# Kernel optimization log

Hardware: AMD Instinct MI355X
Metric: run time of the kernel (lower is better)

Reference implementation:

```python
import jax, jax.numpy as jnp
import numpy as np

S = 15      # subject_nums
C = 2048    # in_channels (extractor output dim)
NC = 3      # num_classes
B = 1024    # subject_batch_num (rows per subject)
SUBJ = 7    # target subject
KERNEL_MUL = 2.0
KERNEL_NUM = 5


def setup_inputs() -> dict:
    key = jax.random.key(0)
    k = jax.random.split(key, 5)
    x = jax.random.normal(k[0], (S * B, C), dtype=jnp.float32)
    labels = jax.random.randint(k[1], (S * B,), 0, NC)
    y = jax.nn.one_hot(labels, NC, dtype=jnp.float32)
    subject_label = jnp.repeat(jnp.arange(S, dtype=jnp.int32), B)
    W_add = 0.02 * jax.random.normal(k[2], (S, 512, C), dtype=jnp.float32)
    b_add = jnp.zeros((S, 512), dtype=jnp.float32)
    W_cls = 0.02 * jax.random.normal(k[3], (S, NC, 512), dtype=jnp.float32)
    b_cls = jnp.zeros((S, NC), dtype=jnp.float32)
    return {"x": x, "y": y, "subject_label": subject_label,
            "W_add": W_add, "b_add": b_add, "W_cls": W_cls, "b_cls": b_cls,
            "subject": SUBJ}


def _mmd(source, target):
    # Standard multi-kernel Gaussian MMD (DAN-style), as used in the repo.
    n = source.shape[0]
    total = jnp.concatenate([source, target], axis=0)      # [2n, d]
    sq = jnp.sum(total * total, axis=-1)
    d2 = sq[:, None] + sq[None, :] - 2.0 * (total @ total.T)  # [2n, 2n]
    m = 2 * n
    bandwidth = jnp.sum(d2) / (m * m - m)
    bandwidth = bandwidth / (KERNEL_MUL ** (KERNEL_NUM // 2))
    kernels = sum(jnp.exp(-d2 / (bandwidth * (KERNEL_MUL ** i))) for i in range(KERNEL_NUM))
    XX = kernels[:n, :n]
    YY = kernels[n:, n:]
    XY = kernels[:n, n:]
    YX = kernels[n:, :n]
    return jnp.mean(XX + YY - XY - YX)


def reference(x, y, subject_label, W_add, b_add, W_cls, b_cls, subject):
    S_ = W_add.shape[0]
    b = x.shape[0] // S_          # == (subject_label == subject).sum() by construction
    K = S_ - 1
    idx = np.array([i for i in range(S_) if i != subject])  # static: subject is a Python int

    xr = x.reshape(S_, b, -1)
    src = xr[idx]                 # [K, b, C] source-subject blocks
    tgt = xr[subject]             # [b, C] target-subject block
    Wk, bk = W_add[idx], b_add[idx]

    # Grouped per-subject addblock Linear(C -> 512)
    outs = jnp.einsum('kbc,kdc->kbd', src, Wk) + bk[:, None, :]       # [K, b, 512]
    t_outs = jnp.einsum('bc,kdc->kbd', tgt, Wk) + bk[:, None, :]      # [K, b, 512]

    # Class predictors: ReLU + Linear(512 -> NC), predictors 0..K-1 are used
    Wc, bc = W_cls[:K], b_cls[:K]
    logits = jnp.einsum('kbd,knd->kbn', jax.nn.relu(outs), Wc) + bc[:, None, :]
    t_logits = jnp.einsum('kbd,knd->kbn', jax.nn.relu(t_outs), Wc) + bc[:, None, :]

    # ---- MMD loss ----
    mmd_loss = jnp.mean(jax.vmap(_mmd)(outs, t_outs))

    # ---- DISC loss: pairwise |softmax - softmax| over source features ----
    P = jax.nn.softmax(outs, axis=-1)                                  # [K, b, 512]
    disc_loss = 0.0
    for i in range(K - 1):  # fixed small loop over subjects, inner term vectorized
        disc_loss = disc_loss + jnp.abs(P[i + 1:] - P[i]).mean(axis=(1, 2)).sum()
    disc_loss = disc_loss * 2.0 / (K * (K - 1))

    # ---- CLS loss: KL(one-hot/soft target || log_softmax(logits)) ----
    yr = y.reshape(S_, b, -1)[idx]                                     # [K, b, NC]
    logp = jax.nn.log_softmax(logits, axis=-1)
    safe_y = jnp.where(yr > 0, yr, 1.0)
    kl = jnp.where(yr > 0, yr * (jnp.log(safe_y) - logp), 0.0)         # 0*log0 -> 0 (torch kl_div)
    cls_loss = kl.sum(-1).mean()

    # ---- PRED ACC on target subject ----
    t_prob = jax.nn.softmax(t_logits, axis=-1).mean(axis=0)            # [b, NC]
    y_tgt = y.reshape(S_, b, -1)[subject]
    pred = jnp.sum(jnp.argmax(t_prob, axis=1) == jnp.argmax(y_tgt, axis=1))
    nums = b

    return (mmd_loss * 0.1, disc_loss * 0.4, cls_loss, pred, nums)
```

## Files before the change

kernel.cpp:

```cpp
#include <hip/hip_runtime.h>
#include <hip/hip_bf16.h>
#include <stdint.h>

typedef __attribute__((ext_vector_type(8))) __bf16 bf16x8;
typedef __attribute__((ext_vector_type(4))) float f32x4;

#define CDIM 2048
#define DDIM 512

__device__ __forceinline__ unsigned short f2bf(float f) {
  union { float f; unsigned u; } a; a.f = f;
  unsigned r = a.u + 0x7FFFu + ((a.u >> 16) & 1u);
  return (unsigned short)(r >> 16);
}
__device__ __forceinline__ float bf2f(unsigned short h) {
  union { unsigned u; float f; } a; a.u = ((unsigned)h) << 16;
  return a.f;
}

typedef const __attribute__((address_space(1))) void gas_void;
typedef __attribute__((address_space(3))) void las_void;
__device__ __forceinline__ void async16(const void* g, void* l) {
  __builtin_amdgcn_global_load_lds((gas_void*)g, (las_void*)l, 16, 0, 0);
}

__device__ __forceinline__ float blockSum256(float v) {
  __shared__ float sh[4];
  #pragma unroll
  for (int o = 32; o; o >>= 1) v += __shfl_xor(v, o, 64);
  int lane = threadIdx.x & 63, w = threadIdx.x >> 6;
  __syncthreads();
  if (lane == 0) sh[w] = v;
  __syncthreads();
  return sh[0] + sh[1] + sh[2] + sh[3];
}

__global__ __launch_bounds__(256) void k_convert(const float* __restrict__ x,
    const float* __restrict__ w, uint2* __restrict__ x16, uint2* __restrict__ w16) {
  const int nx4 = 15*1024*CDIM/4;
  const int nw4 = 15*DDIM*CDIM/4;
  int stride = gridDim.x * blockDim.x;
  for (int i = blockIdx.x*blockDim.x + threadIdx.x; i < nx4; i += stride) {
    float4 v = ((const float4*)x)[i];
    x16[i] = make_uint2((unsigned)f2bf(v.x) | ((unsigned)f2bf(v.y) << 16),
                        (unsigned)f2bf(v.z) | ((unsigned)f2bf(v.w) << 16));
  }
  for (int i = blockIdx.x*blockDim.x + threadIdx.x; i < nw4; i += stride) {
    float4 v = ((const float4*)w)[i];
    w16[i] = make_uint2((unsigned)f2bf(v.x) | ((unsigned)f2bf(v.y) << 16),
                        (unsigned)f2bf(v.z) | ((unsigned)f2bf(v.w) << 16));
  }
}

__global__ __launch_bounds__(256) void k_gemm1(
    const unsigned short* __restrict__ x16,
    const unsigned short* __restrict__ w16,
    const float* __restrict__ b_add,
    const int* __restrict__ subj_p,
    unsigned short* __restrict__ t16)
{
  const int subj = *subj_p;
  int bid = blockIdx.x;
  int k  = bid >> 6;
  int t  = bid & 63;
  int mt = t >> 2, nt = t & 3;
  int ik = (k < subj) ? k : (k + 1);

  __shared__ unsigned short As[128*64];
  __shared__ unsigned short Bs[128*64];

  int tid = threadIdx.x;
  int lane = tid & 63;
  int w = tid >> 6;
  int wm = w >> 1, wn = w & 1;
  int rlane = lane >> 3;
  int col8  = (lane & 7) << 3;

  const unsigned short* Bbase = w16 + (size_t)ik * DDIM * CDIM;

  f32x4 acc[4][4];
  #pragma unroll
  for (int a = 0; a < 4; a++)
    #pragma unroll
    for (int b = 0; b < 4; b++) acc[a][b] = f32x4{0.f,0.f,0.f,0.f};

  for (int ks = 0; ks < CDIM; ks += 64) {
    #pragma unroll
    for (int i = 0; i < 4; i++) {
      int c = w*4 + i;
      int r = c*8 + rlane;
      int gr = mt*128 + r;
      int xrow = ((gr < 1024) ? ik : subj) * 1024 + (gr & 1023);
      async16(x16 + (size_t)xrow*CDIM + ks + col8, (char*)As + c*1024);
      int gn = nt*128 + r;
      async16(Bbase + (size_t)gn*CDIM + ks + col8, (char*)Bs + c*1024);
    }
    __syncthreads();
    #pragma unroll
    for (int kk = 0; kk < 64; kk += 32) {
      bf16x8 af[4], bfr[4];
      #pragma unroll
      for (int a = 0; a < 4; a++)
        af[a] = *(const bf16x8*)(As + (wm*64 + a*16 + (lane & 15))*64 + kk + ((lane >> 4) << 3));
      #pragma unroll
      for (int b = 0; b < 4; b++)
        bfr[b] = *(const bf16x8*)(Bs + (wn*64 + b*16 + (lane & 15))*64 + kk + ((lane >> 4) << 3));
      #pragma unroll
      for (int a = 0; a < 4; a++)
        #pragma unroll
        for (int b = 0; b < 4; b++)
          acc[a][b] = __builtin_amdgcn_mfma_f32_16x16x32_bf16(af[a], bfr[b], acc[a][b], 0, 0, 0);
    }
    __syncthreads();
  }
  const float* bias = b_add + ik*DDIM;
  #pragma unroll
  for (int b = 0; b < 4; b++) {
    int coln = nt*128 + wn*64 + b*16 + (lane & 15);
    float bv = bias[coln];
    #pragma unroll
    for (int a = 0; a < 4; a++) {
      #pragma unroll
      for (int r = 0; r < 4; r++) {
        int rowm = mt*128 + wm*64 + a*16 + ((lane >> 4) << 2) + r;
        t16[((size_t)k*2048 + rowm)*DDIM + coln] = f2bf(acc[a][b][r] + bv);
      }
    }
  }
}

__global__ __launch_bounds__(256) void k_rowred(const unsigned short* __restrict__ t16,
    float* __restrict__ sq, float* __restrict__ rmax, float* __restrict__ rinv)
{
  int wid = blockIdx.x*4 + (threadIdx.x >> 6);
  int lane = threadIdx.x & 63;
  uint4 v = *(const uint4*)(t16 + (size_t)wid * DDIM + lane*8);
  unsigned uu[4] = {v.x, v.y, v.z, v.w};
  float f[8];
  #pragma unroll
  for (int q = 0; q < 4; q++) {
    f[2*q]   = bf2f((unsigned short)(uu[q] & 0xffffu));
    f[2*q+1] = bf2f((unsigned short)(uu[q] >> 16));
  }
  float s2 = 0.f, mx = -3.4e38f;
  #pragma unroll
  for (int j = 0; j < 8; j++) { s2 += f[j]*f[j]; mx = fmaxf(mx, f[j]); }
  #pragma unroll
  for (int o = 32; o; o >>= 1) { s2 += __shfl_xor(s2, o, 64); mx = fmaxf(mx, __shfl_xor(mx, o, 64)); }
  float se = 0.f;
  #pragma unroll
  for (int j = 0; j < 8; j++) se += __expf(f[j] - mx);
  #pragma unroll
  for (int o = 32; o; o >>= 1) se += __shfl_xor(se, o, 64);
  if (lane == 0) { sq[wid] = s2; rmax[wid] = mx; rinv[wid] = 1.f/se; }
}

__global__ __launch_bounds__(256) void k_colsum(const unsigned short* __restrict__ t16,
    float* __restrict__ scol)
{
  int b = blockIdx.x;
  int k = b >> 4, sub = b & 15;
  int d = ((sub & 1) << 8) + threadIdx.x;
  int r0 = (sub >> 1) << 8;
  const unsigned short* base = t16 + (size_t)k*2048*DDIM;
  float s = 0.f;
  for (int r = r0; r < r0 + 256; r++) s += bf2f(base[(size_t)r*DDIM + d]);
  atomicAdd(&scol[k*DDIM + d], s);
}

__global__ __launch_bounds__(256) void k_bw(const float* __restrict__ sq,
    const float* __restrict__ scol, float* __restrict__ c2)
{
  int k = blockIdx.x;
  float a = 0.f;
  for (int r = threadIdx.x; r < 2048; r += 256) a += sq[k*2048 + r];
  float b = 0.f;
  for (int d = threadIdx.x; d < 512; d += 256) { float v = scol[k*512 + d]; b += v*v; }
  float atot = blockSum256(a);
  float btot = blockSum256(b);
  if (threadIdx.x == 0) {
    float sumd2 = 2.f*2048.f*atot - 2.f*btot;
    float bw = sumd2 / (2048.f*2048.f - 2048.f) * 0.25f;
    #pragma unroll
    for (int i = 0; i < 5; i++)
      c2[k*5 + i] = -1.4426950408889634f / (bw * (float)(1 << i));
  }
}

__global__ __launch_bounds__(256) void k_mmd(
    const unsigned short* __restrict__ t16,
    const float* __restrict__ sq,
    const float* __restrict__ c2,
    float* __restrict__ mmdacc)
{
  int bid = blockIdx.x;
  int k = bid / 136;
  int tri = bid - k*136;
  int it = 0;
  while (tri >= 16 - it) { tri -= 16 - it; it++; }
  int jt = it + tri;

  const unsigned short* T = t16 + (size_t)k * 2048 * DDIM;

  __shared__ unsigned short As[128*64];
  __shared__ unsigned short Bs[128*64];
  __shared__ float sqs[256];

  int tid = threadIdx.x;
  int lane = tid & 63;
  int w = tid >> 6;
  int wm = w >> 1, wn = w & 1;
  int rlane = lane >> 3;
  int col8  = (lane & 7) << 3;

  f32x4 acc[4][4];
  #pragma unroll
  for (int a = 0; a < 4; a++)
    #pragma unroll
    for (int b = 0; b < 4; b++) acc[a][b] = f32x4{0.f,0.f,0.f,0.f};

  for (int ks = 0; ks < DDIM; ks += 64) {
    #pragma unroll
    for (int i = 0; i < 4; i++) {
      int c = w*4 + i;
      int r = c*8 + rlane;
      async16(T + (size_t)(it*128 + r)*DDIM + ks + col8, (char*)As + c*1024);
      async16(T + (size_t)(jt*128 + r)*DDIM + ks + col8, (char*)Bs + c*1024);
    }
    __syncthreads();
    #pragma unroll
    for (int kk = 0; kk < 64; kk += 32) {
      bf16x8 af[4], bfr[4];
      #pragma unroll
      for (int a = 0; a < 4; a++)
        af[a] = *(const bf16x8*)(As + (wm*64 + a*16 + (lane & 15))*64 + kk + ((lane >> 4) << 3));
      #pragma unroll
      for (int b = 0; b < 4; b++)
        bfr[b] = *(const bf16x8*)(Bs + (wn*64 + b*16 + (lane & 15))*64 + kk + ((lane >> 4) << 3));
      #pragma unroll
      for (int a = 0; a < 4; a++)
        #pragma unroll
        for (int b = 0; b < 4; b++)
          acc[a][b] = __builtin_amdgcn_mfma_f32_16x16x32_bf16(af[a], bfr[b], acc[a][b], 0, 0, 0);
    }
    __syncthreads();
  }
  if (tid < 128) sqs[tid] = sq[k*2048 + it*128 + tid];
  else           sqs[tid] = sq[k*2048 + jt*128 + (tid - 128)];
  __syncthreads();

  float c0 = c2[k*5], c1 = c2[k*5+1], cA = c2[k*5+2], c3 = c2[k*5+3], c4 = c2[k*5+4];
  float part = 0.f;
  #pragma unroll
  for (int a = 0; a < 4; a++) {
    #pragma unroll
    for (int b = 0; b < 4; b++) {
      int rj = wn*64 + b*16 + (lane & 15);
      float sj = sqs[128 + rj];
      #pragma unroll
      for (int r = 0; r < 4; r++) {
        int ri = wm*64 + a*16 + ((lane >> 4) << 2) + r;
        float d2 = sqs[ri] + sj - 2.f*acc[a][b][r];
        part += exp2f(c0*d2) + exp2f(c1*d2) + exp2f(cA*d2) + exp2f(c3*d2) + exp2f(c4*d2);
      }
    }
  }
  float tot = blockSum256(part);
  if (tid == 0) {
    float sgn = ((it < 8) == (jt < 8)) ? 1.f : -1.f;
    float wgt = (it == jt) ? 1.f : 2.f;
    atomicAdd(&mmdacc[k], sgn * wgt * tot);
  }
}

__global__ __launch_bounds__(256) void k_disc(const unsigned short* __restrict__ t16,
    const float* __restrict__ rmax, const float* __restrict__ rinv, float* __restrict__ discacc)
{
  int b = blockIdx.x;
  int row = b >> 1;
  int d = ((b & 1) << 8) + threadIdx.x;
  float p[14];
  #pragma unroll
  for (int k = 0; k < 14; k++) {
    float tv = bf2f(t16[((size_t)(k*2048 + row))*DDIM + d]);
    p[k] = __expf(tv - rmax[k*2048 + row]) * rinv[k*2048 + row];
  }
  float s = 0.f;
  #pragma unroll
  for (int i2 = 0; i2 < 14; i2++)
    #pragma unroll
    for (int j2 = i2+1; j2 < 14; j2++)
      s += fabsf(p[i2] - p[j2]);
  float tot = blockSum256(s);
  if (threadIdx.x == 0) atomicAdd(discacc, tot);
}

__global__ __launch_bounds__(256) void k_logits(const unsigned short* __restrict__ t16,
    const float* __restrict__ W_cls, const float* __restrict__ b_cls,
    float* __restrict__ logits)
{
  int wid = blockIdx.x*4 + (threadIdx.x >> 6);
  int lane = threadIdx.x & 63;
  int k = wid >> 11;
  uint4 v = *(const uint4*)(t16 + (size_t)wid * DDIM + lane*8);
  unsigned uu[4] = {v.x, v.y, v.z, v.w};
  float f[8];
  #pragma unroll
  for (int q = 0; q < 4; q++) {
    f[2*q]   = fmaxf(bf2f((unsigned short)(uu[q] & 0xffffu)), 0.f);
    f[2*q+1] = fmaxf(bf2f((unsigned short)(uu[q] >> 16)), 0.f);
  }
  const float* Wc = W_cls + k*3*DDIM;
  int d0 = lane*8;
  float l0 = 0.f, l1 = 0.f, l2 = 0.f;
  #pragma unroll
  for (int j = 0; j < 8; j++) {
    l0 += f[j]*Wc[d0+j];
    l1 += f[j]*Wc[DDIM + d0+j];
    l2 += f[j]*Wc[2*DDIM + d0+j];
  }
  #pragma unroll
  for (int o = 32; o; o >>= 1) {
    l0 += __shfl_xor(l0, o, 64); l1 += __shfl_xor(l1, o, 64); l2 += __shfl_xor(l2, o, 64);
  }
  if (lane == 0) {
    logits[(size_t)wid*3 + 0] = l0 + b_cls[k*3 + 0];
    logits[(size_t)wid*3 + 1] = l1 + b_cls[k*3 + 1];
    logits[(size_t)wid*3 + 2] = l2 + b_cls[k*3 + 2];
  }
}

__global__ __launch_bounds__(256) void k_cls(const float* __restrict__ logits,
    const float* __restrict__ y, const int* __restrict__ subj_p, float* __restrict__ clsacc)
{
  int i = blockIdx.x*256 + threadIdx.x;
  int k = i >> 10, r = i & 1023;
  int subj = *subj_p;
  int ik = (k < subj) ? k : k+1;
  const float* l = logits + ((size_t)(k*2048 + r))*3;
  float l0 = l[0], l1 = l[1], l2 = l[2];
  float mx = fmaxf(l0, fmaxf(l1, l2));
  float lse = mx + __logf(__expf(l0-mx) + __expf(l1-mx) + __expf(l2-mx));
  const float* yr = y + ((size_t)(ik*1024 + r))*3;
  float tl = (yr[0] > 0.5f) ? l0 : ((yr[1] > 0.5f) ? l1 : l2);
  float tot = blockSum256(lse - tl);
  if (threadIdx.x == 0) atomicAdd(clsacc, tot);
}

__global__ __launch_bounds__(256) void k_pred(const float* __restrict__ logits,
    const float* __restrict__ y, const int* __restrict__ subj_p, float* __restrict__ predacc)
{
  int j = blockIdx.x*256 + threadIdx.x;
  int subj = *subj_p;
  float p0 = 0.f, p1 = 0.f, p2 = 0.f;
  for (int k = 0; k < 14; k++) {
    const float* l = logits + ((size_t)(k*2048 + 1024 + j))*3;
    float l0 = l[0], l1 = l[1], l2 = l[2];
    float mx = fmaxf(l0, fmaxf(l1, l2));
    float e0 = __expf(l0-mx), e1 = __expf(l1-mx), e2 = __expf(l2-mx);
    float inv = 1.f/(e0+e1+e2);
    p0 += e0*inv; p1 += e1*inv; p2 += e2*inv;
  }
  int pa = 0; float pm = p0;
  if (p1 > pm) { pa = 1; pm = p1; }
  if (p2 > pm) { pa = 2; }
  const float* yt = y + ((size_t)(subj*1024 + j))*3;
  int ya = 0; float ym = yt[0];
  if (yt[1] > ym) { ya = 1; ym = yt[1]; }
  if (yt[2] > ym) { ya = 2; }
  float tot = blockSum256((pa == ya) ? 1.f : 0.f);
  if (threadIdx.x == 0) atomicAdd(predacc, tot);
}

__global__ void k_fin(const float* __restrict__ acc, float* __restrict__ out)
{
  if (threadIdx.x == 0 && blockIdx.x == 0) {
    float s = 0.f;
    for (int k = 0; k < 14; k++) s += acc[k];
    out[0] = 0.1f * s / (14.f * 1024.f * 1024.f);
    out[1] = 0.4f * acc[14] * (2.f / (14.f*13.f)) / (1024.f*512.f);
    out[2] = acc[15] / (14.f*1024.f);
    out[3] = acc[16];
    out[4] = 1024.f;
  }
}

extern "C" void kernel_launch(void* const* d_in, const int* in_sizes, int n_in,
                              void* d_out, int out_size, void* d_ws, size_t ws_size,
                              hipStream_t stream)
{
  (void)in_sizes; (void)n_in; (void)out_size; (void)ws_size;
  const float* x     = (const float*)d_in[0];
  const float* y     = (const float*)d_in[1];
  const float* W_add = (const float*)d_in[3];
  const float* b_add = (const float*)d_in[4];
  const float* W_cls = (const float*)d_in[5];
  const float* b_cls = (const float*)d_in[6];
  const int*   subj  = (const int*)d_in[7];

  char* ws = (char*)d_ws;
  size_t o = 0;
  auto take = [&](size_t b) { char* p = ws + o; o += (b + 255) & ~(size_t)255; return p; };
  unsigned short* X16 = (unsigned short*)take((size_t)15*1024*2048*2);
  unsigned short* W16 = (unsigned short*)take((size_t)15*512*2048*2);
  unsigned short* T16 = (unsigned short*)take((size_t)14*2048*512*2);
  float* SQ   = (float*)take((size_t)14*2048*4);
  float* RMAX = (float*)take((size_t)14*2048*4);
  float* RINV = (float*)take((size_t)14*2048*4);
  float* SCOL = (float*)take((size_t)14*512*4);
  float* C2   = (float*)take(512);
  float* LOG  = (float*)take((size_t)14*2048*3*4);
  float* ACC  = (float*)take(256);

  hipMemsetAsync(SCOL, 0, 14*512*4, stream);
  hipMemsetAsync(ACC, 0, 256, stream);

  k_convert<<<2048, 256, 0, stream>>>(x, W_add, (uint2*)X16, (uint2*)W16);
  k_gemm1 <<<14*64, 256, 0, stream>>>(X16, W16, b_add, subj, T16);
  k_rowred<<<14*2048/4, 256, 0, stream>>>(T16, SQ, RMAX, RINV);
  k_colsum<<<14*16, 256, 0, stream>>>(T16, SCOL);
  k_bw    <<<14, 256, 0, stream>>>(SQ, SCOL, C2);
  k_mmd   <<<14*136, 256, 0, stream>>>(T16, SQ, C2, ACC);
  k_disc  <<<2048, 256, 0, stream>>>(T16, RMAX, RINV, ACC + 14);
  k_logits<<<14*2048/4, 256, 0, stream>>>(T16, W_cls, b_cls, LOG);
  k_cls   <<<56, 256, 0, stream>>>(LOG, y, subj, ACC + 15);
  k_pred  <<<4, 256, 0, stream>>>(LOG, y, subj, ACC + 16);
  k_fin   <<<1, 64, 0, stream>>>(ACC, (float*)d_out);
}
```

Baseline: 509.8 us.

## Swizzle LDS tiles and fuse colsum, disc, logits, cls and pred kernels

Applies an XOR swizzle to the LDS tile layout in both MFMA GEMM kernels to cut bank conflicts on fragment reads. It also folds the column-sum into the row-reduction kernel through shared-memory partials and atomics. The disc, logits, cls and partial pred work are merged into one heads kernel with spread-out accumulators, and the workspace memsets are combined into one. This removes several launches and the round trip of logits through memory, at the cost of many more atomics (scol per block, pacc per row).

```diff
diff --git a/kernel.cpp b/kernel.cpp
--- a/kernel.cpp
+++ b/kernel.cpp
@@ -33,6 +33,10 @@
   if (lane == 0) sh[w] = v;
   __syncthreads();
   return sh[0] + sh[1] + sh[2] + sh[3];
+}
+
+__device__ __forceinline__ bf16x8 lds_frag(const unsigned short* base, int row, int cb) {
+  return *(const bf16x8*)(base + row*64 + (((cb ^ (row & 7))) << 3));
 }
 
 __global__ __launch_bounds__(256) void k_convert(const float* __restrict__ x,
@@ -74,7 +78,7 @@
   int w = tid >> 6;
   int wm = w >> 1, wn = w & 1;
   int rlane = lane >> 3;
-  int col8  = (lane & 7) << 3;
+  int col8  = ((lane & 7) ^ rlane) << 3;
 
   const unsigned short* Bbase = w16 + (size_t)ik * DDIM * CDIM;
 
@@ -101,10 +105,10 @@
       bf16x8 af[4], bfr[4];
       #pragma unroll
       for (int a = 0; a < 4; a++)
-        af[a] = *(const bf16x8*)(As + (wm*64 + a*16 + (lane & 15))*64 + kk + ((lane >> 4) << 3));
+        af[a] = lds_frag(As, wm*64 + a*16 + (lane & 15), (kk >> 3) + (lane >> 4));
       #pragma unroll
       for (int b = 0; b < 4; b++)
-        bfr[b] = *(const bf16x8*)(Bs + (wn*64 + b*16 + (lane & 15))*64 + kk + ((lane >> 4) << 3));
+        bfr[b] = lds_frag(Bs, wn*64 + b*16 + (lane & 15), (kk >> 3) + (lane >> 4));
       #pragma unroll
       for (int a = 0; a < 4; a++)
         #pragma unroll
@@ -130,10 +134,15 @@
 }
 
 __global__ __launch_bounds__(256) void k_rowred(const unsigned short* __restrict__ t16,
-    float* __restrict__ sq, float* __restrict__ rmax, float* __restrict__ rinv)
-{
-  int wid = blockIdx.x*4 + (threadIdx.x >> 6);
-  int lane = threadIdx.x & 63;
+    float* __restrict__ sq, float* __restrict__ rmax, float* __restrict__ rinv,
+    float* __restrict__ scol)
+{
+  __shared__ float cs[4][512];
+  int tidx = threadIdx.x;
+  int w = tidx >> 6;
+  int lane = tidx & 63;
+  int wid = blockIdx.x*4 + w;
+  int k = wid >> 11;
   uint4 v = *(const uint4*)(t16 + (size_t)wid * DDIM + lane*8);
   unsigned uu[4] = {v.x, v.y, v.z, v.w};
   float f[8];
@@ -153,19 +162,11 @@
   #pragma unroll
   for (int o = 32; o; o >>= 1) se += __shfl_xor(se, o, 64);
   if (lane == 0) { sq[wid] = s2; rmax[wid] = mx; rinv[wid] = 1.f/se; }
-}
-
-__global__ __launch_bounds__(256) void k_colsum(const unsigned short* __restrict__ t16,
-    float* __restrict__ scol)
-{
-  int b = blockIdx.x;
-  int k = b >> 4, sub = b & 15;
-  int d = ((sub & 1) << 8) + threadIdx.x;
-  int r0 = (sub >> 1) << 8;
-  const unsigned short* base = t16 + (size_t)k*2048*DDIM;
-  float s = 0.f;
-  for (int r = r0; r < r0 + 256; r++) s += bf2f(base[(size_t)r*DDIM + d]);
-  atomicAdd(&scol[k*DDIM + d], s);
+  #pragma unroll
+  for (int j = 0; j < 8; j++) cs[w][lane*8 + j] = f[j];
+  __syncthreads();
+  atomicAdd(&scol[k*512 + tidx],       cs[0][tidx]     + cs[1][tidx]     + cs[2][tidx]     + cs[3][tidx]);
+  atomicAdd(&scol[k*512 + 256 + tidx], cs[0][tidx+256] + cs[1][tidx+256] + cs[2][tidx+256] + cs[3][tidx+256]);
 }
 
 __global__ __launch_bounds__(256) void k_bw(const float* __restrict__ sq,
@@ -191,7 +192,7 @@
     const unsigned short* __restrict__ t16,
     const float* __restrict__ sq,
     const float* __restrict__ c2,
-    float* __restrict__ mmdacc)
+    float* __restrict__ g_acc)
 {
   int bid = blockIdx.x;
   int k = bid / 136;
@@ -211,7 +212,7 @@
   int w = tid >> 6;
   int wm = w >> 1, wn = w & 1;
   int rlane = lane >> 3;
-  int col8  = (lane & 7) << 3;
+  int col8  = ((lane & 7) ^ rlane) << 3;
 
   f32x4 acc[4][4];
   #pragma unroll
@@ -233,10 +234,10 @@
       bf16x8 af[4], bfr[4];
       #pragma unroll
       for (int a = 0; a < 4; a++)
-        af[a] = *(const bf16x8*)(As + (wm*64 + a*16 + (lane & 15))*64 + kk + ((lane >> 4) << 3));
+        af[a] = lds_frag(As, wm*64 + a*16 + (lane & 15), (kk >> 3) + (lane >> 4));
       #pragma unroll
       for (int b = 0; b < 4; b++)
-        bfr[b] = *(const bf16x8*)(Bs + (wn*64 + b*16 + (lane & 15))*64 + kk + ((lane >> 4) << 3));
+        bfr[b] = lds_frag(Bs, wn*64 + b*16 + (lane & 15), (kk >> 3) + (lane >> 4));
       #pragma unroll
       for (int a = 0; a < 4; a++)
         #pragma unroll
@@ -269,98 +270,99 @@
   if (tid == 0) {
     float sgn = ((it < 8) == (jt < 8)) ? 1.f : -1.f;
     float wgt = (it == jt) ? 1.f : 2.f;
-    atomicAdd(&mmdacc[k], sgn * wgt * tot);
-  }
-}
-
-__global__ __launch_bounds__(256) void k_disc(const unsigned short* __restrict__ t16,
-    const float* __restrict__ rmax, const float* __restrict__ rinv, float* __restrict__ discacc)
-{
-  int b = blockIdx.x;
-  int row = b >> 1;
-  int d = ((b & 1) << 8) + threadIdx.x;
-  float p[14];
-  #pragma unroll
-  for (int k = 0; k < 14; k++) {
-    float tv = bf2f(t16[((size_t)(k*2048 + row))*DDIM + d]);
-    p[k] = __expf(tv - rmax[k*2048 + row]) * rinv[k*2048 + row];
-  }
-  float s = 0.f;
-  #pragma unroll
-  for (int i2 = 0; i2 < 14; i2++)
-    #pragma unroll
-    for (int j2 = i2+1; j2 < 14; j2++)
-      s += fabsf(p[i2] - p[j2]);
-  float tot = blockSum256(s);
-  if (threadIdx.x == 0) atomicAdd(discacc, tot);
-}
-
-__global__ __launch_bounds__(256) void k_logits(const unsigned short* __restrict__ t16,
+    atomicAdd(&g_acc[k], sgn * wgt * tot);
+  }
+}
+
+__global__ __launch_bounds__(256) void k_heads(const unsigned short* __restrict__ t16,
+    const float* __restrict__ rmax, const float* __restrict__ rinv,
     const float* __restrict__ W_cls, const float* __restrict__ b_cls,
-    float* __restrict__ logits)
-{
-  int wid = blockIdx.x*4 + (threadIdx.x >> 6);
-  int lane = threadIdx.x & 63;
-  int k = wid >> 11;
-  uint4 v = *(const uint4*)(t16 + (size_t)wid * DDIM + lane*8);
-  unsigned uu[4] = {v.x, v.y, v.z, v.w};
-  float f[8];
-  #pragma unroll
-  for (int q = 0; q < 4; q++) {
-    f[2*q]   = fmaxf(bf2f((unsigned short)(uu[q] & 0xffffu)), 0.f);
-    f[2*q+1] = fmaxf(bf2f((unsigned short)(uu[q] >> 16)), 0.f);
-  }
-  const float* Wc = W_cls + k*3*DDIM;
-  int d0 = lane*8;
-  float l0 = 0.f, l1 = 0.f, l2 = 0.f;
-  #pragma unroll
-  for (int j = 0; j < 8; j++) {
-    l0 += f[j]*Wc[d0+j];
-    l1 += f[j]*Wc[DDIM + d0+j];
-    l2 += f[j]*Wc[2*DDIM + d0+j];
-  }
-  #pragma unroll
-  for (int o = 32; o; o >>= 1) {
-    l0 += __shfl_xor(l0, o, 64); l1 += __shfl_xor(l1, o, 64); l2 += __shfl_xor(l2, o, 64);
-  }
-  if (lane == 0) {
-    logits[(size_t)wid*3 + 0] = l0 + b_cls[k*3 + 0];
-    logits[(size_t)wid*3 + 1] = l1 + b_cls[k*3 + 1];
-    logits[(size_t)wid*3 + 2] = l2 + b_cls[k*3 + 2];
-  }
-}
-
-__global__ __launch_bounds__(256) void k_cls(const float* __restrict__ logits,
-    const float* __restrict__ y, const int* __restrict__ subj_p, float* __restrict__ clsacc)
-{
-  int i = blockIdx.x*256 + threadIdx.x;
-  int k = i >> 10, r = i & 1023;
-  int subj = *subj_p;
-  int ik = (k < subj) ? k : k+1;
-  const float* l = logits + ((size_t)(k*2048 + r))*3;
-  float l0 = l[0], l1 = l[1], l2 = l[2];
-  float mx = fmaxf(l0, fmaxf(l1, l2));
-  float lse = mx + __logf(__expf(l0-mx) + __expf(l1-mx) + __expf(l2-mx));
-  const float* yr = y + ((size_t)(ik*1024 + r))*3;
-  float tl = (yr[0] > 0.5f) ? l0 : ((yr[1] > 0.5f) ? l1 : l2);
-  float tot = blockSum256(lse - tl);
-  if (threadIdx.x == 0) atomicAdd(clsacc, tot);
-}
-
-__global__ __launch_bounds__(256) void k_pred(const float* __restrict__ logits,
-    const float* __restrict__ y, const int* __restrict__ subj_p, float* __restrict__ predacc)
+    const float* __restrict__ y, const int* __restrict__ subj_p,
+    float* __restrict__ g_acc, float* __restrict__ pacc)
+{
+  if (blockIdx.x < 2048) {
+    int b = blockIdx.x;
+    int row = b >> 1;
+    int d = ((b & 1) << 8) + threadIdx.x;
+    float p[14];
+    #pragma unroll
+    for (int k = 0; k < 14; k++) {
+      float tv = bf2f(t16[((size_t)(k*2048 + row))*DDIM + d]);
+      p[k] = __expf(tv - rmax[k*2048 + row]) * rinv[k*2048 + row];
+    }
+    float s = 0.f;
+    #pragma unroll
+    for (int i2 = 0; i2 < 14; i2++)
+      #pragma unroll
+      for (int j2 = i2+1; j2 < 14; j2++)
+        s += fabsf(p[i2] - p[j2]);
+    float tot = blockSum256(s);
+    if (threadIdx.x == 0) atomicAdd(&g_acc[14 + (b & 7)], tot);
+  } else {
+    __shared__ float shk[4];
+    int bid = blockIdx.x - 2048;
+    int w = threadIdx.x >> 6;
+    int lane = threadIdx.x & 63;
+    int wid = bid*4 + w;
+    int k = wid >> 11, r = wid & 2047;
+    uint4 v = *(const uint4*)(t16 + (size_t)wid * DDIM + lane*8);
+    unsigned uu[4] = {v.x, v.y, v.z, v.w};
+    float f[8];
+    #pragma unroll
+    for (int q = 0; q < 4; q++) {
+      f[2*q]   = fmaxf(bf2f((unsigned short)(uu[q] & 0xffffu)), 0.f);
+      f[2*q+1] = fmaxf(bf2f((unsigned short)(uu[q] >> 16)), 0.f);
+    }
+    const float* Wc = W_cls + k*3*DDIM;
+    int d0 = lane*8;
+    float l0 = 0.f, l1 = 0.f, l2 = 0.f;
+    #pragma unroll
+    for (int j = 0; j < 8; j++) {
+      l0 += f[j]*Wc[d0+j];
+      l1 += f[j]*Wc[DDIM + d0+j];
+      l2 += f[j]*Wc[2*DDIM + d0+j];
+    }
+    #pragma unroll
+    for (int o = 32; o; o >>= 1) {
+      l0 += __shfl_xor(l0, o, 64); l1 += __shfl_xor(l1, o, 64); l2 += __shfl_xor(l2, o, 64);
+    }
+    if (r < 1024) {
+      float kl = 0.f;
+      if (lane == 0) {
+        l0 += b_cls[k*3+0]; l1 += b_cls[k*3+1]; l2 += b_cls[k*3+2];
+        float mx = fmaxf(l0, fmaxf(l1, l2));
+        float lse = mx + __logf(__expf(l0-mx) + __expf(l1-mx) + __expf(l2-mx));
+        int subj = *subj_p;
+        int ik = (k < subj) ? k : k+1;
+        const float* yr = y + ((size_t)(ik*1024 + r))*3;
+        float tl = (yr[0] > 0.5f) ? l0 : ((yr[1] > 0.5f) ? l1 : l2);
+        kl = lse - tl;
+        shk[w] = kl;
+      }
+      __syncthreads();
+      if (threadIdx.x == 0)
+        atomicAdd(&g_acc[22 + k], shk[0] + shk[1] + shk[2] + shk[3]);
+    } else {
+      if (lane == 0) {
+        l0 += b_cls[k*3+0]; l1 += b_cls[k*3+1]; l2 += b_cls[k*3+2];
+        float mx = fmaxf(l0, fmaxf(l1, l2));
+        float e0 = __expf(l0-mx), e1 = __expf(l1-mx), e2 = __expf(l2-mx);
+        float inv = 1.f/(e0+e1+e2);
+        int j = r - 1024;
+        atomicAdd(&pacc[j*3 + 0], e0*inv);
+        atomicAdd(&pacc[j*3 + 1], e1*inv);
+        atomicAdd(&pacc[j*3 + 2], e2*inv);
+      }
+    }
+  }
+}
+
+__global__ __launch_bounds__(256) void k_pred(const float* __restrict__ pacc,
+    const float* __restrict__ y, const int* __restrict__ subj_p, float* __restrict__ g_acc)
 {
   int j = blockIdx.x*256 + threadIdx.x;
   int subj = *subj_p;
-  float p0 = 0.f, p1 = 0.f, p2 = 0.f;
-  for (int k = 0; k < 14; k++) {
-    const float* l = logits + ((size_t)(k*2048 + 1024 + j))*3;
-    float l0 = l[0], l1 = l[1], l2 = l[2];
-    float mx = fmaxf(l0, fmaxf(l1, l2));
-    float e0 = __expf(l0-mx), e1 = __expf(l1-mx), e2 = __expf(l2-mx);
-    float inv = 1.f/(e0+e1+e2);
-    p0 += e0*inv; p1 += e1*inv; p2 += e2*inv;
-  }
+  float p0 = pacc[j*3+0], p1 = pacc[j*3+1], p2 = pacc[j*3+2];
   int pa = 0; float pm = p0;
   if (p1 > pm) { pa = 1; pm = p1; }
   if (p2 > pm) { pa = 2; }
@@ -369,18 +371,22 @@
   if (yt[1] > ym) { ya = 1; ym = yt[1]; }
   if (yt[2] > ym) { ya = 2; }
   float tot = blockSum256((pa == ya) ? 1.f : 0.f);
-  if (threadIdx.x == 0) atomicAdd(predacc, tot);
-}
-
-__global__ void k_fin(const float* __restrict__ acc, float* __restrict__ out)
+  if (threadIdx.x == 0) atomicAdd(&g_acc[36], tot);
+}
+
+__global__ void k_fin(const float* __restrict__ g_acc, float* __restrict__ out)
 {
   if (threadIdx.x == 0 && blockIdx.x == 0) {
     float s = 0.f;
-    for (int k = 0; k < 14; k++) s += acc[k];
+    for (int k = 0; k < 14; k++) s += g_acc[k];
+    float disc = 0.f;
+    for (int i = 14; i < 22; i++) disc += g_acc[i];
+    float cls = 0.f;
+    for (int i = 22; i < 36; i++) cls += g_acc[i];
     out[0] = 0.1f * s / (14.f * 1024.f * 1024.f);
-    out[1] = 0.4f * acc[14] * (2.f / (14.f*13.f)) / (1024.f*512.f);
-    out[2] = acc[15] / (14.f*1024.f);
-    out[3] = acc[16];
+    out[1] = 0.4f * disc * (2.f / (14.f*13.f)) / (1024.f*512.f);
+    out[2] = cls / (14.f*1024.f);
+    out[3] = g_acc[36];
     out[4] = 1024.f;
   }
 }
@@ -407,23 +413,19 @@
   float* SQ   = (float*)take((size_t)14*2048*4);
   float* RMAX = (float*)take((size_t)14*2048*4);
   float* RINV = (float*)take((size_t)14*2048*4);
+  float* C2   = (float*)take(512);
   float* SCOL = (float*)take((size_t)14*512*4);
-  float* C2   = (float*)take(512);
-  float* LOG  = (float*)take((size_t)14*2048*3*4);
+  float* PACC = (float*)take((size_t)1024*3*4);
   float* ACC  = (float*)take(256);
 
-  hipMemsetAsync(SCOL, 0, 14*512*4, stream);
-  hipMemsetAsync(ACC, 0, 256, stream);
+  hipMemsetAsync(SCOL, 0, 14*512*4 + 1024*3*4 + 256, stream);
 
   k_convert<<<2048, 256, 0, stream>>>(x, W_add, (uint2*)X16, (uint2*)W16);
   k_gemm1 <<<14*64, 256, 0, stream>>>(X16, W16, b_add, subj, T16);
-  k_rowred<<<14*2048/4, 256, 0, stream>>>(T16, SQ, RMAX, RINV);
-  k_colsum<<<14*16, 256, 0, stream>>>(T16, SCOL);
+  k_rowred<<<14*2048/4, 256, 0, stream>>>(T16, SQ, RMAX, RINV, SCOL);
   k_bw    <<<14, 256, 0, stream>>>(SQ, SCOL, C2);
   k_mmd   <<<14*136, 256, 0, stream>>>(T16, SQ, C2, ACC);
-  k_disc  <<<2048, 256, 0, stream>>>(T16, RMAX, RINV, ACC + 14);
-  k_logits<<<14*2048/4, 256, 0, stream>>>(T16, W_cls, b_cls, LOG);
-  k_cls   <<<56, 256, 0, stream>>>(LOG, y, subj, ACC + 15);
-  k_pred  <<<4, 256, 0, stream>>>(LOG, y, subj, ACC + 16);
+  k_heads <<<2048 + 14*2048/4, 256, 0, stream>>>(T16, RMAX, RINV, W_cls, b_cls, y, subj, ACC, PACC);
+  k_pred  <<<4, 256, 0, stream>>>(PACC, y, subj, ACC);
   k_fin   <<<1, 64, 0, stream>>>(ACC, (float*)d_out);
 }
```

Measured after the change: 527.5 us. 3.5% more time.
